# Kernel optimization log

Hardware: AMD Instinct MI355X
Metric: run time of the kernel (lower is better)

The kernel has to match this reference:

```python
import jax, jax.numpy as jnp
import numpy as np

EPS = 1e-08

def setup_inputs() -> dict:
    key = jax.random.key(0)
    k1, k2, k3, k4 = jax.random.split(key, 4)
    B, N, IN, OUT, WF = 16, 4096, 512, 512, 512
    x = jax.random.normal(k1, (B, N, IN), dtype=jnp.float32)
    w = jax.random.normal(k2, (B, WF), dtype=jnp.float32)
    # kaiming-normal-like init for the main weight
    weight = jax.random.normal(k3, (OUT, IN), dtype=jnp.float32) * np.sqrt(2.0 / IN)
    bias = jnp.zeros((OUT,), dtype=jnp.float32)
    A_w = jax.random.normal(k4, (IN, WF), dtype=jnp.float32) * np.sqrt(1.0 / WF)
    A_b = jnp.zeros((IN,), dtype=jnp.float32)
    return {"x": x, "w": w, "weight": weight, "bias": bias, "A_w": A_w, "A_b": A_b}

def reference(x, w, weight, bias, A_w, A_b):
    # style -> per-input-channel scale: (B, in)
    s = w @ A_w.T + A_b
    # modulate: (B, out, in)
    wm = weight[None, :, :] * s[:, None, :]
    # demodulate: rsqrt over in-dim
    norm = jax.lax.rsqrt(EPS + jnp.sum(wm * wm, axis=2, keepdims=True))
    wd = wm * norm
    # batched matmul: (B, N, in) x (B, out, in) -> (B, N, out)
    out = jnp.einsum('bni,boi->bno', x, wd) + bias
    return jax.nn.relu(out)
```

## Files before the change

### kernel.cpp

```cpp
#include <hip/hip_runtime.h>
#include <hip/hip_bf16.h>

#define B_    16
#define M_    4096
#define K_    512
#define O_    512

#define BM 128
#define BN 128
#define BK 32

typedef float f32x4 __attribute__((ext_vector_type(4)));
typedef short bf16x8 __attribute__((ext_vector_type(8)));
typedef unsigned short u16x8 __attribute__((ext_vector_type(8)));

__device__ __forceinline__ int chunk_off(int row, int kq) {
    return (row * 4 + (kq ^ ((row >> 1) & 3))) * 8;
}

__global__ void style_kernel(const float* __restrict__ w, const float* __restrict__ A_w,
                             const float* __restrict__ A_b, float* __restrict__ s) {
    int b = blockIdx.x;
    int i = blockIdx.y * 64 + threadIdx.x;
    __shared__ float wsh[512];
    for (int j = threadIdx.x; j < 512; j += 64) wsh[j] = w[b * 512 + j];
    __syncthreads();
    const float* arow = A_w + (size_t)i * 512;
    float acc = 0.f;
    #pragma unroll 4
    for (int f = 0; f < 512; f += 4) {
        float4 a = *(const float4*)(arow + f);
        acc += a.x * wsh[f] + a.y * wsh[f + 1] + a.z * wsh[f + 2] + a.w * wsh[f + 3];
    }
    s[b * 512 + i] = acc + A_b[i];
}

__global__ void nrm_kernel(const float* __restrict__ weight, const float* __restrict__ s,
                           float* __restrict__ nrm) {
    int gw = blockIdx.x * 4 + (threadIdx.x >> 6);
    int lane = threadIdx.x & 63;
    int b = gw >> 9;
    int o = gw & 511;
    const float* wrow = weight + (size_t)o * 512;
    const float* srow = s + b * 512;
    float ss = 0.f;
    #pragma unroll
    for (int j = 0; j < 8; j++) {
        int i = lane + j * 64;
        float v = wrow[i] * srow[i];
        ss += v * v;
    }
    #pragma unroll
    for (int off = 32; off; off >>= 1) ss += __shfl_xor(ss, off);
    if (lane == 0) nrm[b * 512 + o] = rsqrtf(1e-8f + ss);
}

__global__ void wcast_kernel(const float* __restrict__ weight, unsigned short* __restrict__ wb) {
    int e = (blockIdx.x * 256 + threadIdx.x) * 4;
    float4 v = *(const float4*)(weight + e);
    union { __hip_bfloat162 h[2]; unsigned long long u; } cv;
    cv.h[0] = __float22bfloat162_rn(float2{v.x, v.y});
    cv.h[1] = __float22bfloat162_rn(float2{v.z, v.w});
    *(unsigned long long*)(wb + e) = cv.u;
}

__global__ __launch_bounds__(256, 4) void gemm_kernel(const float* __restrict__ x,
                                                      const unsigned short* __restrict__ wb,
                                                      const float* __restrict__ s,
                                                      const float* __restrict__ nrm,
                                                      const float* __restrict__ bias,
                                                      float* __restrict__ out) {
    __shared__ unsigned short sA[2][BM * BK];
    __shared__ unsigned short sB[2][BN * BK];
    __shared__ float sS[K_];

    int g = blockIdx.x;
    int xcd = g & 7;
    int grp = g >> 3;
    int nblk = grp & 3;
    int mb = xcd * 64 + (grp >> 2);
    const int b  = mb >> 5;
    const int m0 = (mb & 31) * BM;
    const int n0 = nblk * BN;

    const float* xb = x + (size_t)b * M_ * K_;

    const int t = threadIdx.x;
    const int w = t >> 6;
    const int l = t & 63;
    const int wave_row = (w >> 1) * 64;
    const int wave_col = (w & 1) * 64;
    const int lrow  = l & 15;
    const int kq_l  = l >> 4;

    *(float2*)(&sS[t * 2]) = *(const float2*)(s + b * K_ + t * 2);

    int offA[4], offB[4];
    #pragma unroll
    for (int mi = 0; mi < 4; mi++) offA[mi] = chunk_off(wave_row + mi * 16 + lrow, kq_l);
    #pragma unroll
    for (int ni = 0; ni < 4; ni++) offB[ni] = chunk_off(wave_col + ni * 16 + lrow, kq_l);

    const int ar = t >> 1;
    const int aq = t & 1;
    const float* abase = xb + (size_t)(m0 + ar) * K_ + aq * 16;
    const unsigned short* bbase = wb + (size_t)(n0 + ar) * K_ + aq * 16;

    f32x4 araw[4];
    u16x8 braw[2];
    #pragma unroll
    for (int j = 0; j < 4; j++) araw[j] = *(const f32x4*)(abase + j * 4);
    #pragma unroll
    for (int j = 0; j < 2; j++) braw[j] = *(const u16x8*)(bbase + j * 8);

    __syncthreads();

    f32x4 acc[4][4] = {};

    #pragma unroll 2
    for (int i = 0; i < 16; i++) {
        const int kk = i * BK;
        const int buf = i & 1;

        #pragma unroll
        for (int j = 0; j < 2; j++) {
            f32x4 s0 = *(const f32x4*)(&sS[kk + aq * 16 + j * 8]);
            f32x4 s1 = *(const f32x4*)(&sS[kk + aq * 16 + j * 8 + 4]);
            f32x4 p0 = araw[2 * j] * s0;
            f32x4 p1 = araw[2 * j + 1] * s1;
            union { __hip_bfloat162 h[4]; u16x8 v; } cv;
            cv.h[0] = __float22bfloat162_rn(float2{p0[0], p0[1]});
            cv.h[1] = __float22bfloat162_rn(float2{p0[2], p0[3]});
            cv.h[2] = __float22bfloat162_rn(float2{p1[0], p1[1]});
            cv.h[3] = __float22bfloat162_rn(float2{p1[2], p1[3]});
            *(u16x8*)(&sA[buf][chunk_off(ar, aq * 2 + j)]) = cv.v;
        }
        #pragma unroll
        for (int j = 0; j < 2; j++)
            *(u16x8*)(&sB[buf][chunk_off(ar, aq * 2 + j)]) = braw[j];

        if (i < 15) {
            #pragma unroll
            for (int j = 0; j < 4; j++) araw[j] = *(const f32x4*)(abase + kk + BK + j * 4);
            #pragma unroll
            for (int j = 0; j < 2; j++) braw[j] = *(const u16x8*)(bbase + kk + BK + j * 8);
        }

        __syncthreads();

        bf16x8 af[4], bfr[4];
        #pragma unroll
        for (int mi = 0; mi < 4; mi++) af[mi] = *(const bf16x8*)(&sA[buf][offA[mi]]);
        #pragma unroll
        for (int ni = 0; ni < 4; ni++) bfr[ni] = *(const bf16x8*)(&sB[buf][offB[ni]]);
        #pragma unroll
        for (int mi = 0; mi < 4; mi++)
            #pragma unroll
            for (int ni = 0; ni < 4; ni++)
                acc[mi][ni] = __builtin_amdgcn_mfma_f32_16x16x32_bf16(af[mi], bfr[ni], acc[mi][ni], 0, 0, 0);
    }

    const int col_l = l & 15;
    const int row_q = (l >> 4) * 4;
    #pragma unroll
    for (int ni = 0; ni < 4; ni++) {
        int o = n0 + wave_col + ni * 16 + col_l;
        float bv = bias[o];
        float nv = nrm[b * 512 + o];
        #pragma unroll
        for (int mi = 0; mi < 4; mi++) {
            int mrow = m0 + wave_row + mi * 16 + row_q;
            #pragma unroll
            for (int r = 0; r < 4; r++) {
                float v = acc[mi][ni][r] * nv + bv;
                out[((size_t)b * M_ + mrow + r) * O_ + o] = v > 0.f ? v : 0.f;
            }
        }
    }
}

extern "C" void kernel_launch(void* const* d_in, const int* in_sizes, int n_in,
                              void* d_out, int out_size, void* d_ws, size_t ws_size,
                              hipStream_t stream) {
    const float* x      = (const float*)d_in[0];
    const float* w      = (const float*)d_in[1];
    const float* weight = (const float*)d_in[2];
    const float* bias   = (const float*)d_in[3];
    const float* A_w    = (const float*)d_in[4];
    const float* A_b    = (const float*)d_in[5];
    float* out = (float*)d_out;

    unsigned short* wbf = (unsigned short*)d_ws;
    float* s   = (float*)((char*)d_ws + 512 * 1024);
    float* nrm = (float*)((char*)d_ws + 512 * 1024 + 32 * 1024);

    style_kernel<<<dim3(B_, 8), 64, 0, stream>>>(w, A_w, A_b, s);
    wcast_kernel<<<(O_ * K_) / 1024, 256, 0, stream>>>(weight, wbf);
    nrm_kernel<<<(B_ * O_) / 4, 256, 0, stream>>>(weight, s, nrm);
    gemm_kernel<<<2048, 256, 0, stream>>>(x, wbf, s, nrm, bias, out);
}
```

Before: 315.4 us.

## Deepen GEMM prefetch to two stages and overlap LDS writes with MFMA

Restructures the GEMM main loop so global loads for tile i+2 are issued into a two-deep register buffer while MFMAs run on tile i. The next tile's scale, convert and LDS store happen after the MFMAs, leaving one barrier per iteration. The barrier becomes a custom macro that waits only on LDS counters, so outstanding global loads need not drain. This uses more registers for the extra prefetch stage, which may lower occupancy under launch_bounds(256,4).

```diff
diff --git a/kernel.cpp b/kernel.cpp
--- a/kernel.cpp
+++ b/kernel.cpp
@@ -13,6 +13,11 @@
 typedef float f32x4 __attribute__((ext_vector_type(4)));
 typedef short bf16x8 __attribute__((ext_vector_type(8)));
 typedef unsigned short u16x8 __attribute__((ext_vector_type(8)));
+
+#define LDS_BARRIER() do { \
+    __builtin_amdgcn_s_waitcnt(0xC07F); \
+    __builtin_amdgcn_s_barrier(); \
+} while (0)
 
 __device__ __forceinline__ int chunk_off(int row, int kq) {
     return (row * 4 + (kq ^ ((row >> 1) & 3))) * 8;
@@ -93,8 +98,6 @@
     const int lrow  = l & 15;
     const int kq_l  = l >> 4;
 
-    *(float2*)(&sS[t * 2]) = *(const float2*)(s + b * K_ + t * 2);
-
     int offA[4], offB[4];
     #pragma unroll
     for (int mi = 0; mi < 4; mi++) offA[mi] = chunk_off(wave_row + mi * 16 + lrow, kq_l);
@@ -105,59 +108,86 @@
     const int aq = t & 1;
     const float* abase = xb + (size_t)(m0 + ar) * K_ + aq * 16;
     const unsigned short* bbase = wb + (size_t)(n0 + ar) * K_ + aq * 16;
-
-    f32x4 araw[4];
-    u16x8 braw[2];
-    #pragma unroll
-    for (int j = 0; j < 4; j++) araw[j] = *(const f32x4*)(abase + j * 4);
-    #pragma unroll
-    for (int j = 0; j < 2; j++) braw[j] = *(const u16x8*)(bbase + j * 8);
-
-    __syncthreads();
-
-    f32x4 acc[4][4] = {};
-
-    #pragma unroll 2
-    for (int i = 0; i < 16; i++) {
-        const int kk = i * BK;
-        const int buf = i & 1;
-
+    const int wr_off0 = chunk_off(ar, aq * 2);
+    const int wr_off1 = chunk_off(ar, aq * 2 + 1);
+
+    f32x4 araw[2][4];
+    u16x8 braw[2][2];
+
+    #pragma unroll
+    for (int st = 0; st < 2; st++) {
+        #pragma unroll
+        for (int j = 0; j < 4; j++) araw[st][j] = *(const f32x4*)(abase + st * BK + j * 4);
+        #pragma unroll
+        for (int j = 0; j < 2; j++) braw[st][j] = *(const u16x8*)(bbase + st * BK + j * 8);
+    }
+    *(float2*)(&sS[t * 2]) = *(const float2*)(s + b * K_ + t * 2);
+    LDS_BARRIER();
+
+    {
         #pragma unroll
         for (int j = 0; j < 2; j++) {
-            f32x4 s0 = *(const f32x4*)(&sS[kk + aq * 16 + j * 8]);
-            f32x4 s1 = *(const f32x4*)(&sS[kk + aq * 16 + j * 8 + 4]);
-            f32x4 p0 = araw[2 * j] * s0;
-            f32x4 p1 = araw[2 * j + 1] * s1;
+            f32x4 s0 = *(const f32x4*)(&sS[aq * 16 + j * 8]);
+            f32x4 s1 = *(const f32x4*)(&sS[aq * 16 + j * 8 + 4]);
+            f32x4 p0 = araw[0][2 * j] * s0;
+            f32x4 p1 = araw[0][2 * j + 1] * s1;
             union { __hip_bfloat162 h[4]; u16x8 v; } cv;
             cv.h[0] = __float22bfloat162_rn(float2{p0[0], p0[1]});
             cv.h[1] = __float22bfloat162_rn(float2{p0[2], p0[3]});
             cv.h[2] = __float22bfloat162_rn(float2{p1[0], p1[1]});
             cv.h[3] = __float22bfloat162_rn(float2{p1[2], p1[3]});
-            *(u16x8*)(&sA[buf][chunk_off(ar, aq * 2 + j)]) = cv.v;
-        }
-        #pragma unroll
-        for (int j = 0; j < 2; j++)
-            *(u16x8*)(&sB[buf][chunk_off(ar, aq * 2 + j)]) = braw[j];
-
-        if (i < 15) {
-            #pragma unroll
-            for (int j = 0; j < 4; j++) araw[j] = *(const f32x4*)(abase + kk + BK + j * 4);
-            #pragma unroll
-            for (int j = 0; j < 2; j++) braw[j] = *(const u16x8*)(bbase + kk + BK + j * 8);
-        }
-
-        __syncthreads();
+            *(u16x8*)(&sA[0][j == 0 ? wr_off0 : wr_off1]) = cv.v;
+        }
+        *(u16x8*)(&sB[0][wr_off0]) = braw[0][0];
+        *(u16x8*)(&sB[0][wr_off1]) = braw[0][1];
+    }
+    LDS_BARRIER();
+
+    f32x4 acc[4][4] = {};
+
+    #pragma unroll 2
+    for (int i = 0; i < 16; i++) {
+        const int buf = i & 1;
 
         bf16x8 af[4], bfr[4];
         #pragma unroll
         for (int mi = 0; mi < 4; mi++) af[mi] = *(const bf16x8*)(&sA[buf][offA[mi]]);
         #pragma unroll
         for (int ni = 0; ni < 4; ni++) bfr[ni] = *(const bf16x8*)(&sB[buf][offB[ni]]);
+
+        if (i < 14) {
+            #pragma unroll
+            for (int j = 0; j < 4; j++) araw[buf][j] = *(const f32x4*)(abase + (i + 2) * BK + j * 4);
+            #pragma unroll
+            for (int j = 0; j < 2; j++) braw[buf][j] = *(const u16x8*)(bbase + (i + 2) * BK + j * 8);
+        }
+
         #pragma unroll
         for (int mi = 0; mi < 4; mi++)
             #pragma unroll
             for (int ni = 0; ni < 4; ni++)
                 acc[mi][ni] = __builtin_amdgcn_mfma_f32_16x16x32_bf16(af[mi], bfr[ni], acc[mi][ni], 0, 0, 0);
+
+        if (i < 15) {
+            const int nb = buf ^ 1;
+            const int kk1 = (i + 1) * BK;
+            #pragma unroll
+            for (int j = 0; j < 2; j++) {
+                f32x4 s0 = *(const f32x4*)(&sS[kk1 + aq * 16 + j * 8]);
+                f32x4 s1 = *(const f32x4*)(&sS[kk1 + aq * 16 + j * 8 + 4]);
+                f32x4 p0 = araw[nb][2 * j] * s0;
+                f32x4 p1 = araw[nb][2 * j + 1] * s1;
+                union { __hip_bfloat162 h[4]; u16x8 v; } cv;
+                cv.h[0] = __float22bfloat162_rn(float2{p0[0], p0[1]});
+                cv.h[1] = __float22bfloat162_rn(float2{p0[2], p0[3]});
+                cv.h[2] = __float22bfloat162_rn(float2{p1[0], p1[1]});
+                cv.h[3] = __float22bfloat162_rn(float2{p1[2], p1[3]});
+                *(u16x8*)(&sA[nb][j == 0 ? wr_off0 : wr_off1]) = cv.v;
+            }
+            *(u16x8*)(&sB[nb][wr_off0]) = braw[nb][0];
+            *(u16x8*)(&sB[nb][wr_off1]) = braw[nb][1];
+            LDS_BARRIER();
+        }
     }
 
     const int col_l = l & 15;
```

Result: slower. 417.5 us (+32.4%).
